# Kernel optimization log

Hardware: AMD Instinct MI355X
Metric: run time of the kernel (lower is better)

## Reference

```python
import jax, jax.numpy as jnp
import numpy as np

INPUT_DIM = 64
RESERVOIR_DIM = 2048
OUTPUT_DIM = 64
SPECTRAL_RADIUS = 0.9
LEAK_RATE = 0.3
SPARSITY = 0.9
INPUT_SCALING = 1.0
NOISE_LEVEL = 0.01
T = 4096


def setup_inputs() -> dict:
    key = jax.random.key(0)
    k_u, k_n = jax.random.split(key)
    u = jax.random.normal(k_u, (T, INPUT_DIM), dtype=jnp.float32)
    noise = jax.random.normal(k_n, (T, RESERVOIR_DIM), dtype=jnp.float32)

    # Reservoir weights, built exactly like the torch __init__ (fixed, untrained).
    rng = np.random.default_rng(0)
    W_in = (rng.standard_normal((RESERVOIR_DIM, INPUT_DIM)) * INPUT_SCALING).astype(np.float32)
    W = (rng.uniform(0.0, 1.0, (RESERVOIR_DIM, RESERVOIR_DIM)) * 2.0 - 1.0).astype(np.float32)
    mask = rng.uniform(0.0, 1.0, (RESERVOIR_DIM, RESERVOIR_DIM)) > SPARSITY
    W = W * mask.astype(np.float32)
    sr = np.max(np.abs(np.linalg.eigvals(W)))  # spectral radius normalization
    W = (W * (SPECTRAL_RADIUS / sr)).astype(np.float32)

    # nn.Linear(reservoir_dim, output_dim) init: U(-1/sqrt(N), 1/sqrt(N))
    bound = 1.0 / np.sqrt(RESERVOIR_DIM)
    readout_w = rng.uniform(-bound, bound, (OUTPUT_DIM, RESERVOIR_DIM)).astype(np.float32)
    readout_b = rng.uniform(-bound, bound, (OUTPUT_DIM,)).astype(np.float32)

    return {
        "u": u,
        "noise": noise,
        "W_in": jnp.asarray(W_in),
        "W": jnp.asarray(W),
        "readout_w": jnp.asarray(readout_w),
        "readout_b": jnp.asarray(readout_b),
    }


def reference(u, noise, W_in, W, readout_w, readout_b):
    # Leaky-integrated ESN recurrence, state reset to zeros (reset_state=True).
    input_terms = u @ W_in.T + noise * NOISE_LEVEL  # [T, N], precompute input GEMM

    def step(state, it):
        new_state = jnp.tanh(it + W @ state)
        state = (1.0 - LEAK_RATE) * state + LEAK_RATE * new_state
        return state, state

    init = jnp.zeros((RESERVOIR_DIM,), dtype=u.dtype)
    _, states = jax.lax.scan(step, init, input_terms)  # states: [T, N]
    return states @ readout_w.T + readout_b  # [T, output_dim]
```

## Files before the change

### kernel.cpp

```cpp
#include <hip/hip_runtime.h>

#define T_STEPS 4096
#define N_RES   2048
#define N_IN    64
#define N_OUT   64
#define LEAK    0.3f
#define NOISE_S 0.01f

#define NWG     128
#define RPW     16
#define RPWAVE  4

typedef unsigned int uint32x4 __attribute__((ext_vector_type(4)));

__global__ __launch_bounds__(256) void input_terms_kernel(
    const float* __restrict__ u, const float* __restrict__ noise,
    const float* __restrict__ W_in, float* __restrict__ it) {
  const int t = blockIdx.x;
  const int tid = threadIdx.x;
  __shared__ float su[N_IN];
  if (tid < N_IN) su[tid] = u[(size_t)t * N_IN + tid];
  __syncthreads();
  #pragma unroll
  for (int k = 0; k < N_RES / 256; ++k) {
    const int n = tid + 256 * k;
    const float4* wr = reinterpret_cast<const float4*>(W_in + (size_t)n * N_IN);
    float acc = 0.f;
    #pragma unroll
    for (int j = 0; j < N_IN / 4; ++j) {
      float4 w4 = wr[j];
      acc = fmaf(w4.x, su[4 * j + 0], acc);
      acc = fmaf(w4.y, su[4 * j + 1], acc);
      acc = fmaf(w4.z, su[4 * j + 2], acc);
      acc = fmaf(w4.w, su[4 * j + 3], acc);
    }
    it[(size_t)t * N_RES + n] = acc + NOISE_S * noise[(size_t)t * N_RES + n];
  }
}

__global__ __launch_bounds__(256, 1) void reservoir_kernel(
    const float* __restrict__ W, float* __restrict__ it,
    unsigned int* sbuf) {
  const int wg = blockIdx.x;
  const int tid = threadIdx.x;
  const int wave = tid >> 6;
  const int lane = tid & 63;
  const int R = wg * RPW;
  const int r0 = R + wave * RPWAVE;

  __shared__ float Wl[RPW * N_RES];
  __shared__ float ls[2][N_RES];

  {
    const float4* Wg = reinterpret_cast<const float4*>(W + (size_t)R * N_RES);
    float4* Wd = reinterpret_cast<float4*>(Wl);
    #pragma unroll
    for (int k = 0; k < RPW * N_RES / 4 / 256; ++k)
      Wd[tid + 256 * k] = Wg[tid + 256 * k];
  }

  float itv = 0.f;
  if (lane < RPWAVE) itv = it[r0 + lane];

  {
    const uint32x4* pa = reinterpret_cast<const uint32x4*>(sbuf) + tid;
    const uint32x4* pb = pa + 256;
    uint32x4* dsta = reinterpret_cast<uint32x4*>(&ls[0][0]) + tid;
    uint32x4* dstb = dsta + 256;
    unsigned int need = 3u;
    while (need) {
      uint32x4 va, vb;
      asm volatile(
          "global_load_dwordx4 %0, %2, off sc0 sc1\n\t"
          "global_load_dwordx4 %1, %3, off sc0 sc1\n\t"
          "s_waitcnt vmcnt(0)"
          : "=&v"(va), "=&v"(vb) : "v"(pa), "v"(pb) : "memory");
      if ((need & 1u) &&
          (((va[0] | va[1] | va[2] | va[3]) & 3u) == 0u)) { *dsta = va; need &= ~1u; }
      if ((need & 2u) &&
          (((vb[0] | vb[1] | vb[2] | vb[3]) & 3u) == 0u)) { *dstb = vb; need &= ~2u; }
      if (need) __builtin_amdgcn_s_sleep(1);
    }
  }
  __syncthreads();

  for (unsigned int t = 0; t < T_STEPS; ++t) {
    const float* cur = ls[t & 1];
    float* nxt = ls[(t + 1) & 1];
    unsigned int* swb = sbuf + ((t + 1) & 1) * N_RES;

    const float4* S4 = reinterpret_cast<const float4*>(cur);
    const float4* W0 = reinterpret_cast<const float4*>(Wl + (size_t)(RPWAVE * wave + 0) * N_RES);
    const float4* W1 = reinterpret_cast<const float4*>(Wl + (size_t)(RPWAVE * wave + 1) * N_RES);
    const float4* W2 = reinterpret_cast<const float4*>(Wl + (size_t)(RPWAVE * wave + 2) * N_RES);
    const float4* W3 = reinterpret_cast<const float4*>(Wl + (size_t)(RPWAVE * wave + 3) * N_RES);
    float a0 = 0.f, a1 = 0.f, a2 = 0.f, a3 = 0.f;
    #pragma unroll
    for (int j = 0; j < N_RES / 4 / 64; ++j) {
      const float4 s4 = S4[lane + 64 * j];
      const float4 x0 = W0[lane + 64 * j];
      const float4 x1 = W1[lane + 64 * j];
      const float4 x2 = W2[lane + 64 * j];
      const float4 x3 = W3[lane + 64 * j];
      a0 = fmaf(x0.x, s4.x, a0); a0 = fmaf(x0.y, s4.y, a0);
      a0 = fmaf(x0.z, s4.z, a0); a0 = fmaf(x0.w, s4.w, a0);
      a1 = fmaf(x1.x, s4.x, a1); a1 = fmaf(x1.y, s4.y, a1);
      a1 = fmaf(x1.z, s4.z, a1); a1 = fmaf(x1.w, s4.w, a1);
      a2 = fmaf(x2.x, s4.x, a2); a2 = fmaf(x2.y, s4.y, a2);
      a2 = fmaf(x2.z, s4.z, a2); a2 = fmaf(x2.w, s4.w, a2);
      a3 = fmaf(x3.x, s4.x, a3); a3 = fmaf(x3.y, s4.y, a3);
      a3 = fmaf(x3.z, s4.z, a3); a3 = fmaf(x3.w, s4.w, a3);
    }
    #pragma unroll
    for (int off = 32; off > 0; off >>= 1) {
      a0 += __shfl_xor(a0, off);
      a1 += __shfl_xor(a1, off);
      a2 += __shfl_xor(a2, off);
      a3 += __shfl_xor(a3, off);
    }

    float snew = 0.f;
    if (lane < RPWAVE) {
      const float a = (lane == 0) ? a0 : (lane == 1) ? a1 : (lane == 2) ? a2 : a3;
      const float h = tanhf(itv + a);
      const float sold = cur[r0 + lane];
      snew = (1.0f - LEAK) * sold + LEAK * h;
      it[(size_t)t * N_RES + r0 + lane] = snew;
    }

    {
      const unsigned int tg = (t + 1) & 3u;
      uint32x4 pk;
      pk[0] = (__float_as_uint(__shfl(snew, 0)) & ~3u) | tg;
      pk[1] = (__float_as_uint(__shfl(snew, 1)) & ~3u) | tg;
      pk[2] = (__float_as_uint(__shfl(snew, 2)) & ~3u) | tg;
      pk[3] = (__float_as_uint(__shfl(snew, 3)) & ~3u) | tg;
      if (lane == 0) {
        uint32x4* dst = reinterpret_cast<uint32x4*>(swb) + (r0 >> 2);
        asm volatile("global_store_dwordx4 %0, %1, off sc0 sc1"
                     :: "v"(dst), "v"(pk) : "memory");
      }
    }

    if (t + 1 < T_STEPS) {
      if (lane < RPWAVE) itv = it[(size_t)(t + 1) * N_RES + r0 + lane];

      const unsigned int tag = (t + 1) & 3u;
      const uint32x4* pa = reinterpret_cast<const uint32x4*>(swb) + tid;
      const uint32x4* pb = pa + 256;
      uint32x4* dsta = reinterpret_cast<uint32x4*>(nxt) + tid;
      uint32x4* dstb = dsta + 256;
      unsigned int need = 3u;
      for (;;) {
        uint32x4 va, vb;
        if (need == 3u) {
          asm volatile(
              "global_load_dwordx4 %0, %2, off sc0 sc1\n\t"
              "global_load_dwordx4 %1, %3, off sc0 sc1\n\t"
              "s_waitcnt vmcnt(0)"
              : "=&v"(va), "=&v"(vb) : "v"(pa), "v"(pb) : "memory");
          if ((((va[0] ^ tag) | (va[1] ^ tag) | (va[2] ^ tag) | (va[3] ^ tag)) & 3u) == 0u) {
            *dsta = va; need &= ~1u;
          }
          if ((((vb[0] ^ tag) | (vb[1] ^ tag) | (vb[2] ^ tag) | (vb[3] ^ tag)) & 3u) == 0u) {
            *dstb = vb; need &= ~2u;
          }
        } else if (need == 1u) {
          asm volatile(
              "global_load_dwordx4 %0, %1, off sc0 sc1\n\t"
              "s_waitcnt vmcnt(0)"
              : "=&v"(va) : "v"(pa) : "memory");
          if ((((va[0] ^ tag) | (va[1] ^ tag) | (va[2] ^ tag) | (va[3] ^ tag)) & 3u) == 0u) {
            *dsta = va; need = 0u;
          }
        } else {
          asm volatile(
              "global_load_dwordx4 %0, %1, off sc0 sc1\n\t"
              "s_waitcnt vmcnt(0)"
              : "=&v"(vb) : "v"(pb) : "memory");
          if ((((vb[0] ^ tag) | (vb[1] ^ tag) | (vb[2] ^ tag) | (vb[3] ^ tag)) & 3u) == 0u) {
            *dstb = vb; need = 0u;
          }
        }
        if (!need) break;
        __builtin_amdgcn_s_sleep(1);
      }
    }
    __syncthreads();
  }
}

__global__ __launch_bounds__(256) void readout_kernel(
    const float* __restrict__ states, const float* __restrict__ rw,
    const float* __restrict__ rb, float* __restrict__ out) {
  const int t = blockIdx.x;
  const int tid = threadIdx.x;
  const int o = tid & 63;
  const int q = tid >> 6;
  __shared__ float ss[N_RES];
  #pragma unroll
  for (int k = 0; k < N_RES / 256; ++k)
    ss[tid + 256 * k] = states[(size_t)t * N_RES + tid + 256 * k];
  __syncthreads();

  const float4* r4 = reinterpret_cast<const float4*>(rw + (size_t)o * N_RES + q * 512);
  float acc = 0.f;
  #pragma unroll 8
  for (int j = 0; j < 128; ++j) {
    float4 w4 = r4[j];
    const int base = q * 512 + 4 * j;
    acc = fmaf(w4.x, ss[base + 0], acc);
    acc = fmaf(w4.y, ss[base + 1], acc);
    acc = fmaf(w4.z, ss[base + 2], acc);
    acc = fmaf(w4.w, ss[base + 3], acc);
  }
  __shared__ float red[256];
  red[tid] = acc;
  __syncthreads();
  if (tid < 64) {
    float v = red[tid] + red[tid + 64] + red[tid + 128] + red[tid + 192];
    out[(size_t)t * N_OUT + tid] = v + rb[tid];
  }
}

extern "C" void kernel_launch(void* const* d_in, const int* in_sizes, int n_in,
                              void* d_out, int out_size, void* d_ws, size_t ws_size,
                              hipStream_t stream) {
  const float* u     = (const float*)d_in[0];
  const float* noise = (const float*)d_in[1];
  const float* W_in  = (const float*)d_in[2];
  const float* W     = (const float*)d_in[3];
  const float* rw    = (const float*)d_in[4];
  const float* rb    = (const float*)d_in[5];
  float* out = (float*)d_out;

  float* it = (float*)d_ws;
  unsigned int* sbuf =
      (unsigned int*)((char*)d_ws + (size_t)T_STEPS * N_RES * sizeof(float));

  hipMemsetAsync(sbuf, 0, 2 * N_RES * sizeof(unsigned int), stream);

  input_terms_kernel<<<T_STEPS, 256, 0, stream>>>(u, noise, W_in, it);

  void* args[] = {(void*)&W, (void*)&it, (void*)&sbuf};
  hipLaunchCooperativeKernel((void*)reservoir_kernel, dim3(NWG), dim3(256),
                             args, 0, stream);

  readout_kernel<<<T_STEPS, 256, 0, stream>>>(it, rw, rb, out);
}
```

Measured before the change: 13.63 ms.

## Add dedicated polling wave to gather peer states while compute waves run

Splits the reservoir workgroup into four compute waves and one extra wave that only polls the global exchange buffer. The poller issues all eight tagged loads per round and copies ready chunks into shared memory. Each compute wave writes its own new state straight into shared memory, so it skips polling its own chunk. The aim is to take the spin-wait off the compute waves and remove the redundant self-fetch. In exchange, one wave is serialized on polling and a block-wide barrier is still needed every step.

```diff
diff --git a/kernel.cpp b/kernel.cpp
--- a/kernel.cpp
+++ b/kernel.cpp
@@ -7,9 +7,10 @@
 #define LEAK    0.3f
 #define NOISE_S 0.01f
 
-#define NWG     128
-#define RPW     16
-#define RPWAVE  4
+#define NWG      128
+#define RPW      16
+#define RPWAVE   4
+#define NTHREADS 320
 
 typedef unsigned int uint32x4 __attribute__((ext_vector_type(4)));
 
@@ -38,7 +39,7 @@
   }
 }
 
-__global__ __launch_bounds__(256, 1) void reservoir_kernel(
+__global__ __launch_bounds__(NTHREADS, 1) void reservoir_kernel(
     const float* __restrict__ W, float* __restrict__ it,
     unsigned int* sbuf) {
   const int wg = blockIdx.x;
@@ -46,7 +47,6 @@
   const int wave = tid >> 6;
   const int lane = tid & 63;
   const int R = wg * RPW;
-  const int r0 = R + wave * RPWAVE;
 
   __shared__ float Wl[RPW * N_RES];
   __shared__ float ls[2][N_RES];
@@ -54,139 +54,124 @@
   {
     const float4* Wg = reinterpret_cast<const float4*>(W + (size_t)R * N_RES);
     float4* Wd = reinterpret_cast<float4*>(Wl);
-    #pragma unroll
-    for (int k = 0; k < RPW * N_RES / 4 / 256; ++k)
-      Wd[tid + 256 * k] = Wg[tid + 256 * k];
-  }
-
-  float itv = 0.f;
-  if (lane < RPWAVE) itv = it[r0 + lane];
-
-  {
-    const uint32x4* pa = reinterpret_cast<const uint32x4*>(sbuf) + tid;
-    const uint32x4* pb = pa + 256;
-    uint32x4* dsta = reinterpret_cast<uint32x4*>(&ls[0][0]) + tid;
-    uint32x4* dstb = dsta + 256;
-    unsigned int need = 3u;
-    while (need) {
-      uint32x4 va, vb;
-      asm volatile(
-          "global_load_dwordx4 %0, %2, off sc0 sc1\n\t"
-          "global_load_dwordx4 %1, %3, off sc0 sc1\n\t"
-          "s_waitcnt vmcnt(0)"
-          : "=&v"(va), "=&v"(vb) : "v"(pa), "v"(pb) : "memory");
-      if ((need & 1u) &&
-          (((va[0] | va[1] | va[2] | va[3]) & 3u) == 0u)) { *dsta = va; need &= ~1u; }
-      if ((need & 2u) &&
-          (((vb[0] | vb[1] | vb[2] | vb[3]) & 3u) == 0u)) { *dstb = vb; need &= ~2u; }
-      if (need) __builtin_amdgcn_s_sleep(1);
-    }
-  }
-  __syncthreads();
-
-  for (unsigned int t = 0; t < T_STEPS; ++t) {
-    const float* cur = ls[t & 1];
-    float* nxt = ls[(t + 1) & 1];
-    unsigned int* swb = sbuf + ((t + 1) & 1) * N_RES;
-
-    const float4* S4 = reinterpret_cast<const float4*>(cur);
+    for (int idx = tid; idx < RPW * N_RES / 4; idx += NTHREADS)
+      Wd[idx] = Wg[idx];
+  }
+  for (int idx = tid; idx < N_RES; idx += NTHREADS) ls[0][idx] = 0.f;
+  __syncthreads();
+
+  if (wave < 4) {
+    const int r0 = R + wave * RPWAVE;
     const float4* W0 = reinterpret_cast<const float4*>(Wl + (size_t)(RPWAVE * wave + 0) * N_RES);
     const float4* W1 = reinterpret_cast<const float4*>(Wl + (size_t)(RPWAVE * wave + 1) * N_RES);
     const float4* W2 = reinterpret_cast<const float4*>(Wl + (size_t)(RPWAVE * wave + 2) * N_RES);
     const float4* W3 = reinterpret_cast<const float4*>(Wl + (size_t)(RPWAVE * wave + 3) * N_RES);
-    float a0 = 0.f, a1 = 0.f, a2 = 0.f, a3 = 0.f;
-    #pragma unroll
-    for (int j = 0; j < N_RES / 4 / 64; ++j) {
-      const float4 s4 = S4[lane + 64 * j];
-      const float4 x0 = W0[lane + 64 * j];
-      const float4 x1 = W1[lane + 64 * j];
-      const float4 x2 = W2[lane + 64 * j];
-      const float4 x3 = W3[lane + 64 * j];
-      a0 = fmaf(x0.x, s4.x, a0); a0 = fmaf(x0.y, s4.y, a0);
-      a0 = fmaf(x0.z, s4.z, a0); a0 = fmaf(x0.w, s4.w, a0);
-      a1 = fmaf(x1.x, s4.x, a1); a1 = fmaf(x1.y, s4.y, a1);
-      a1 = fmaf(x1.z, s4.z, a1); a1 = fmaf(x1.w, s4.w, a1);
-      a2 = fmaf(x2.x, s4.x, a2); a2 = fmaf(x2.y, s4.y, a2);
-      a2 = fmaf(x2.z, s4.z, a2); a2 = fmaf(x2.w, s4.w, a2);
-      a3 = fmaf(x3.x, s4.x, a3); a3 = fmaf(x3.y, s4.y, a3);
-      a3 = fmaf(x3.z, s4.z, a3); a3 = fmaf(x3.w, s4.w, a3);
-    }
-    #pragma unroll
-    for (int off = 32; off > 0; off >>= 1) {
-      a0 += __shfl_xor(a0, off);
-      a1 += __shfl_xor(a1, off);
-      a2 += __shfl_xor(a2, off);
-      a3 += __shfl_xor(a3, off);
-    }
-
-    float snew = 0.f;
-    if (lane < RPWAVE) {
-      const float a = (lane == 0) ? a0 : (lane == 1) ? a1 : (lane == 2) ? a2 : a3;
-      const float h = tanhf(itv + a);
-      const float sold = cur[r0 + lane];
-      snew = (1.0f - LEAK) * sold + LEAK * h;
-      it[(size_t)t * N_RES + r0 + lane] = snew;
-    }
-
-    {
+
+    float itv = 0.f;
+    if (lane < RPWAVE) itv = it[r0 + lane];
+
+    for (unsigned int t = 0; t < T_STEPS; ++t) {
+      const float* cur = ls[t & 1];
+      float* nxt = ls[(t + 1) & 1];
+      unsigned int* swb = sbuf + ((t + 1) & 1) * N_RES;
+
+      const float4* S4 = reinterpret_cast<const float4*>(cur);
+      float a0 = 0.f, a1 = 0.f, a2 = 0.f, a3 = 0.f;
+      #pragma unroll
+      for (int j = 0; j < N_RES / 4 / 64; ++j) {
+        const float4 s4 = S4[lane + 64 * j];
+        const float4 x0 = W0[lane + 64 * j];
+        const float4 x1 = W1[lane + 64 * j];
+        const float4 x2 = W2[lane + 64 * j];
+        const float4 x3 = W3[lane + 64 * j];
+        a0 = fmaf(x0.x, s4.x, a0); a0 = fmaf(x0.y, s4.y, a0);
+        a0 = fmaf(x0.z, s4.z, a0); a0 = fmaf(x0.w, s4.w, a0);
+        a1 = fmaf(x1.x, s4.x, a1); a1 = fmaf(x1.y, s4.y, a1);
+        a1 = fmaf(x1.z, s4.z, a1); a1 = fmaf(x1.w, s4.w, a1);
+        a2 = fmaf(x2.x, s4.x, a2); a2 = fmaf(x2.y, s4.y, a2);
+        a2 = fmaf(x2.z, s4.z, a2); a2 = fmaf(x2.w, s4.w, a2);
+        a3 = fmaf(x3.x, s4.x, a3); a3 = fmaf(x3.y, s4.y, a3);
+        a3 = fmaf(x3.z, s4.z, a3); a3 = fmaf(x3.w, s4.w, a3);
+      }
+      #pragma unroll
+      for (int off = 32; off > 0; off >>= 1) {
+        a0 += __shfl_xor(a0, off);
+        a1 += __shfl_xor(a1, off);
+        a2 += __shfl_xor(a2, off);
+        a3 += __shfl_xor(a3, off);
+      }
+
       const unsigned int tg = (t + 1) & 3u;
+      unsigned int pkw = 0;
+      if (lane < RPWAVE) {
+        const float a = (lane == 0) ? a0 : (lane == 1) ? a1 : (lane == 2) ? a2 : a3;
+        const float h = tanhf(itv + a);
+        const float sold = cur[r0 + lane];
+        const float snew = (1.0f - LEAK) * sold + LEAK * h;
+        pkw = (__float_as_uint(snew) & ~3u) | tg;
+        nxt[r0 + lane] = __uint_as_float(pkw);
+        it[(size_t)t * N_RES + r0 + lane] = snew;
+      }
       uint32x4 pk;
-      pk[0] = (__float_as_uint(__shfl(snew, 0)) & ~3u) | tg;
-      pk[1] = (__float_as_uint(__shfl(snew, 1)) & ~3u) | tg;
-      pk[2] = (__float_as_uint(__shfl(snew, 2)) & ~3u) | tg;
-      pk[3] = (__float_as_uint(__shfl(snew, 3)) & ~3u) | tg;
+      pk[0] = __shfl(pkw, 0);
+      pk[1] = __shfl(pkw, 1);
+      pk[2] = __shfl(pkw, 2);
+      pk[3] = __shfl(pkw, 3);
       if (lane == 0) {
         uint32x4* dst = reinterpret_cast<uint32x4*>(swb) + (r0 >> 2);
         asm volatile("global_store_dwordx4 %0, %1, off sc0 sc1"
                      :: "v"(dst), "v"(pk) : "memory");
       }
-    }
-
-    if (t + 1 < T_STEPS) {
-      if (lane < RPWAVE) itv = it[(size_t)(t + 1) * N_RES + r0 + lane];
-
-      const unsigned int tag = (t + 1) & 3u;
-      const uint32x4* pa = reinterpret_cast<const uint32x4*>(swb) + tid;
-      const uint32x4* pb = pa + 256;
-      uint32x4* dsta = reinterpret_cast<uint32x4*>(nxt) + tid;
-      uint32x4* dstb = dsta + 256;
-      unsigned int need = 3u;
-      for (;;) {
-        uint32x4 va, vb;
-        if (need == 3u) {
+      if (lane < RPWAVE && t + 1 < T_STEPS)
+        itv = it[(size_t)(t + 1) * N_RES + r0 + lane];
+
+      __syncthreads();
+    }
+  } else {
+    unsigned int ownmask = 0;
+    {
+      const int j = lane - ((wg * 4) & 63);
+      if (0 <= j && j < 4) ownmask = 1u << (wg >> 4);
+    }
+    for (unsigned int t = 0; t < T_STEPS; ++t) {
+      if (t + 1 < T_STEPS) {
+        unsigned int* swb = sbuf + ((t + 1) & 1) * N_RES;
+        float* nxt = ls[(t + 1) & 1];
+        const unsigned int tg = (t + 1) & 3u;
+        const char* p0 = (const char*)swb + lane * 16;
+        const char* p1 = p0 + 4096;
+        uint32x4* dst = reinterpret_cast<uint32x4*>(nxt);
+        unsigned int need = 0xFFu & ~ownmask;
+        for (;;) {
+          uint32x4 v0, v1, v2, v3, v4, v5, v6, v7;
           asm volatile(
-              "global_load_dwordx4 %0, %2, off sc0 sc1\n\t"
-              "global_load_dwordx4 %1, %3, off sc0 sc1\n\t"
+              "global_load_dwordx4 %0, %8, off sc0 sc1\n\t"
+              "global_load_dwordx4 %1, %8, off offset:1024 sc0 sc1\n\t"
+              "global_load_dwordx4 %2, %8, off offset:2048 sc0 sc1\n\t"
+              "global_load_dwordx4 %3, %8, off offset:3072 sc0 sc1\n\t"
+              "global_load_dwordx4 %4, %9, off sc0 sc1\n\t"
+              "global_load_dwordx4 %5, %9, off offset:1024 sc0 sc1\n\t"
+              "global_load_dwordx4 %6, %9, off offset:2048 sc0 sc1\n\t"
+              "global_load_dwordx4 %7, %9, off offset:3072 sc0 sc1\n\t"
               "s_waitcnt vmcnt(0)"
-              : "=&v"(va), "=&v"(vb) : "v"(pa), "v"(pb) : "memory");
-          if ((((va[0] ^ tag) | (va[1] ^ tag) | (va[2] ^ tag) | (va[3] ^ tag)) & 3u) == 0u) {
-            *dsta = va; need &= ~1u;
-          }
-          if ((((vb[0] ^ tag) | (vb[1] ^ tag) | (vb[2] ^ tag) | (vb[3] ^ tag)) & 3u) == 0u) {
-            *dstb = vb; need &= ~2u;
-          }
-        } else if (need == 1u) {
-          asm volatile(
-              "global_load_dwordx4 %0, %1, off sc0 sc1\n\t"
-              "s_waitcnt vmcnt(0)"
-              : "=&v"(va) : "v"(pa) : "memory");
-          if ((((va[0] ^ tag) | (va[1] ^ tag) | (va[2] ^ tag) | (va[3] ^ tag)) & 3u) == 0u) {
-            *dsta = va; need = 0u;
-          }
-        } else {
-          asm volatile(
-              "global_load_dwordx4 %0, %1, off sc0 sc1\n\t"
-              "s_waitcnt vmcnt(0)"
-              : "=&v"(vb) : "v"(pb) : "memory");
-          if ((((vb[0] ^ tag) | (vb[1] ^ tag) | (vb[2] ^ tag) | (vb[3] ^ tag)) & 3u) == 0u) {
-            *dstb = vb; need = 0u;
-          }
+              : "=&v"(v0), "=&v"(v1), "=&v"(v2), "=&v"(v3),
+                "=&v"(v4), "=&v"(v5), "=&v"(v6), "=&v"(v7)
+              : "v"(p0), "v"(p1)
+              : "memory");
+          if ((need & 1u)   && ((((v0[0]^tg)|(v0[1]^tg)|(v0[2]^tg)|(v0[3]^tg))&3u)==0u)) { dst[lane +   0] = v0; need &= ~1u; }
+          if ((need & 2u)   && ((((v1[0]^tg)|(v1[1]^tg)|(v1[2]^tg)|(v1[3]^tg))&3u)==0u)) { dst[lane +  64] = v1; need &= ~2u; }
+          if ((need & 4u)   && ((((v2[0]^tg)|(v2[1]^tg)|(v2[2]^tg)|(v2[3]^tg))&3u)==0u)) { dst[lane + 128] = v2; need &= ~4u; }
+          if ((need & 8u)   && ((((v3[0]^tg)|(v3[1]^tg)|(v3[2]^tg)|(v3[3]^tg))&3u)==0u)) { dst[lane + 192] = v3; need &= ~8u; }
+          if ((need & 16u)  && ((((v4[0]^tg)|(v4[1]^tg)|(v4[2]^tg)|(v4[3]^tg))&3u)==0u)) { dst[lane + 256] = v4; need &= ~16u; }
+          if ((need & 32u)  && ((((v5[0]^tg)|(v5[1]^tg)|(v5[2]^tg)|(v5[3]^tg))&3u)==0u)) { dst[lane + 320] = v5; need &= ~32u; }
+          if ((need & 64u)  && ((((v6[0]^tg)|(v6[1]^tg)|(v6[2]^tg)|(v6[3]^tg))&3u)==0u)) { dst[lane + 384] = v6; need &= ~64u; }
+          if ((need & 128u) && ((((v7[0]^tg)|(v7[1]^tg)|(v7[2]^tg)|(v7[3]^tg))&3u)==0u)) { dst[lane + 448] = v7; need &= ~128u; }
+          if (__all(need == 0u)) break;
+          __builtin_amdgcn_s_sleep(1);
         }
-        if (!need) break;
-        __builtin_amdgcn_s_sleep(1);
-      }
-    }
-    __syncthreads();
+      }
+      __syncthreads();
+    }
   }
 }
 
@@ -243,7 +228,7 @@
   input_terms_kernel<<<T_STEPS, 256, 0, stream>>>(u, noise, W_in, it);
 
   void* args[] = {(void*)&W, (void*)&it, (void*)&sbuf};
-  hipLaunchCooperativeKernel((void*)reservoir_kernel, dim3(NWG), dim3(256),
+  hipLaunchCooperativeKernel((void*)reservoir_kernel, dim3(NWG), dim3(NTHREADS),
                              args, 0, stream);
 
   readout_kernel<<<T_STEPS, 256, 0, stream>>>(it, rw, rb, out);
```

New measurement: 13.11 ms. -3.9%, faster.

## Spread recurrence over 256 workgroups and skip polling own state chunk

Applied to the files above, without the earlier changes.

The persistent recurrence kernel now uses 256 workgroups of 8 rows each instead of 128 of 16, so each wave computes 2 rows and the per-step dot product per workgroup is halved. Each workgroup writes its own new state values straight into shared memory and skips polling the global chunk it produced. The initial poll of the global buffer is replaced by zeroing the local state. The price is twice as many workgroups taking part in the per-step global flag exchange, which raises synchronisation traffic and needs all 256 to be co-resident.

```diff
diff --git a/kernel.cpp b/kernel.cpp
--- a/kernel.cpp
+++ b/kernel.cpp
@@ -7,11 +7,12 @@
 #define LEAK    0.3f
 #define NOISE_S 0.01f
 
-#define NWG     128
-#define RPW     16
-#define RPWAVE  4
+#define NWG      256
+#define RPW      8
+#define RPWAVE   2
 
 typedef unsigned int uint32x4 __attribute__((ext_vector_type(4)));
+typedef unsigned int uint32x2 __attribute__((ext_vector_type(2)));
 
 __global__ __launch_bounds__(256) void input_terms_kernel(
     const float* __restrict__ u, const float* __restrict__ noise,
@@ -58,31 +59,18 @@
     for (int k = 0; k < RPW * N_RES / 4 / 256; ++k)
       Wd[tid + 256 * k] = Wg[tid + 256 * k];
   }
+  for (int idx = tid; idx < N_RES; idx += 256) ls[0][idx] = 0.f;
+  __syncthreads();
+
+  const float4* W0 = reinterpret_cast<const float4*>(Wl + (size_t)(RPWAVE * wave + 0) * N_RES);
+  const float4* W1 = reinterpret_cast<const float4*>(Wl + (size_t)(RPWAVE * wave + 1) * N_RES);
+
+  const bool own0 = ((tid >> 1) == wg);
+  const bool own1 = (((tid + 256) >> 1) == wg);
+  const unsigned int own_mask = (own0 ? 1u : 0u) | (own1 ? 2u : 0u);
 
   float itv = 0.f;
   if (lane < RPWAVE) itv = it[r0 + lane];
-
-  {
-    const uint32x4* pa = reinterpret_cast<const uint32x4*>(sbuf) + tid;
-    const uint32x4* pb = pa + 256;
-    uint32x4* dsta = reinterpret_cast<uint32x4*>(&ls[0][0]) + tid;
-    uint32x4* dstb = dsta + 256;
-    unsigned int need = 3u;
-    while (need) {
-      uint32x4 va, vb;
-      asm volatile(
-          "global_load_dwordx4 %0, %2, off sc0 sc1\n\t"
-          "global_load_dwordx4 %1, %3, off sc0 sc1\n\t"
-          "s_waitcnt vmcnt(0)"
-          : "=&v"(va), "=&v"(vb) : "v"(pa), "v"(pb) : "memory");
-      if ((need & 1u) &&
-          (((va[0] | va[1] | va[2] | va[3]) & 3u) == 0u)) { *dsta = va; need &= ~1u; }
-      if ((need & 2u) &&
-          (((vb[0] | vb[1] | vb[2] | vb[3]) & 3u) == 0u)) { *dstb = vb; need &= ~2u; }
-      if (need) __builtin_amdgcn_s_sleep(1);
-    }
-  }
-  __syncthreads();
 
   for (unsigned int t = 0; t < T_STEPS; ++t) {
     const float* cur = ls[t & 1];
@@ -90,100 +78,85 @@
     unsigned int* swb = sbuf + ((t + 1) & 1) * N_RES;
 
     const float4* S4 = reinterpret_cast<const float4*>(cur);
-    const float4* W0 = reinterpret_cast<const float4*>(Wl + (size_t)(RPWAVE * wave + 0) * N_RES);
-    const float4* W1 = reinterpret_cast<const float4*>(Wl + (size_t)(RPWAVE * wave + 1) * N_RES);
-    const float4* W2 = reinterpret_cast<const float4*>(Wl + (size_t)(RPWAVE * wave + 2) * N_RES);
-    const float4* W3 = reinterpret_cast<const float4*>(Wl + (size_t)(RPWAVE * wave + 3) * N_RES);
-    float a0 = 0.f, a1 = 0.f, a2 = 0.f, a3 = 0.f;
-    #pragma unroll
-    for (int j = 0; j < N_RES / 4 / 64; ++j) {
+    float a0 = 0.f, a1 = 0.f;
+    #pragma unroll
+    for (int j = 0; j < 8; ++j) {
       const float4 s4 = S4[lane + 64 * j];
       const float4 x0 = W0[lane + 64 * j];
       const float4 x1 = W1[lane + 64 * j];
-      const float4 x2 = W2[lane + 64 * j];
-      const float4 x3 = W3[lane + 64 * j];
       a0 = fmaf(x0.x, s4.x, a0); a0 = fmaf(x0.y, s4.y, a0);
       a0 = fmaf(x0.z, s4.z, a0); a0 = fmaf(x0.w, s4.w, a0);
       a1 = fmaf(x1.x, s4.x, a1); a1 = fmaf(x1.y, s4.y, a1);
       a1 = fmaf(x1.z, s4.z, a1); a1 = fmaf(x1.w, s4.w, a1);
-      a2 = fmaf(x2.x, s4.x, a2); a2 = fmaf(x2.y, s4.y, a2);
-      a2 = fmaf(x2.z, s4.z, a2); a2 = fmaf(x2.w, s4.w, a2);
-      a3 = fmaf(x3.x, s4.x, a3); a3 = fmaf(x3.y, s4.y, a3);
-      a3 = fmaf(x3.z, s4.z, a3); a3 = fmaf(x3.w, s4.w, a3);
     }
     #pragma unroll
     for (int off = 32; off > 0; off >>= 1) {
       a0 += __shfl_xor(a0, off);
       a1 += __shfl_xor(a1, off);
-      a2 += __shfl_xor(a2, off);
-      a3 += __shfl_xor(a3, off);
-    }
-
+    }
+
+    const unsigned int tg = (t + 1) & 3u;
+    unsigned int pkw = 0;
     float snew = 0.f;
     if (lane < RPWAVE) {
-      const float a = (lane == 0) ? a0 : (lane == 1) ? a1 : (lane == 2) ? a2 : a3;
+      const float a = lane ? a1 : a0;
       const float h = tanhf(itv + a);
       const float sold = cur[r0 + lane];
       snew = (1.0f - LEAK) * sold + LEAK * h;
+      pkw = (__float_as_uint(snew) & ~3u) | tg;
+      nxt[r0 + lane] = __uint_as_float(pkw);
+    }
+    uint32x2 pk;
+    pk[0] = __shfl(pkw, 0);
+    pk[1] = __shfl(pkw, 1);
+    if (lane == 0) {
+      uint32x2* dst = reinterpret_cast<uint32x2*>(swb + r0);
+      asm volatile("global_store_dwordx2 %0, %1, off sc0 sc1"
+                   :: "v"(dst), "v"(pk) : "memory");
+    }
+    if (lane < RPWAVE) {
       it[(size_t)t * N_RES + r0 + lane] = snew;
-    }
-
-    {
-      const unsigned int tg = (t + 1) & 3u;
-      uint32x4 pk;
-      pk[0] = (__float_as_uint(__shfl(snew, 0)) & ~3u) | tg;
-      pk[1] = (__float_as_uint(__shfl(snew, 1)) & ~3u) | tg;
-      pk[2] = (__float_as_uint(__shfl(snew, 2)) & ~3u) | tg;
-      pk[3] = (__float_as_uint(__shfl(snew, 3)) & ~3u) | tg;
-      if (lane == 0) {
-        uint32x4* dst = reinterpret_cast<uint32x4*>(swb) + (r0 >> 2);
-        asm volatile("global_store_dwordx4 %0, %1, off sc0 sc1"
-                     :: "v"(dst), "v"(pk) : "memory");
-      }
+      if (t + 1 < T_STEPS)
+        itv = it[(size_t)(t + 1) * N_RES + r0 + lane];
     }
 
     if (t + 1 < T_STEPS) {
-      if (lane < RPWAVE) itv = it[(size_t)(t + 1) * N_RES + r0 + lane];
-
-      const unsigned int tag = (t + 1) & 3u;
-      const uint32x4* pa = reinterpret_cast<const uint32x4*>(swb) + tid;
-      const uint32x4* pb = pa + 256;
-      uint32x4* dsta = reinterpret_cast<uint32x4*>(nxt) + tid;
-      uint32x4* dstb = dsta + 256;
-      unsigned int need = 3u;
-      for (;;) {
+      const char* p0 = (const char*)swb + tid * 16;
+      const char* p1 = p0 + 4096;
+      uint32x4* nxt16 = reinterpret_cast<uint32x4*>(nxt);
+      unsigned int need = 3u & ~own_mask;
+      while (need) {
         uint32x4 va, vb;
         if (need == 3u) {
           asm volatile(
               "global_load_dwordx4 %0, %2, off sc0 sc1\n\t"
               "global_load_dwordx4 %1, %3, off sc0 sc1\n\t"
               "s_waitcnt vmcnt(0)"
-              : "=&v"(va), "=&v"(vb) : "v"(pa), "v"(pb) : "memory");
-          if ((((va[0] ^ tag) | (va[1] ^ tag) | (va[2] ^ tag) | (va[3] ^ tag)) & 3u) == 0u) {
-            *dsta = va; need &= ~1u;
-          }
-          if ((((vb[0] ^ tag) | (vb[1] ^ tag) | (vb[2] ^ tag) | (vb[3] ^ tag)) & 3u) == 0u) {
-            *dstb = vb; need &= ~2u;
+              : "=&v"(va), "=&v"(vb) : "v"(p0), "v"(p1) : "memory");
+          if ((((va[0] ^ tg) | (va[1] ^ tg) | (va[2] ^ tg) | (va[3] ^ tg)) & 3u) == 0u) {
+            nxt16[tid] = va; need &= ~1u;
+          }
+          if ((((vb[0] ^ tg) | (vb[1] ^ tg) | (vb[2] ^ tg) | (vb[3] ^ tg)) & 3u) == 0u) {
+            nxt16[tid + 256] = vb; need &= ~2u;
           }
         } else if (need == 1u) {
           asm volatile(
               "global_load_dwordx4 %0, %1, off sc0 sc1\n\t"
               "s_waitcnt vmcnt(0)"
-              : "=&v"(va) : "v"(pa) : "memory");
-          if ((((va[0] ^ tag) | (va[1] ^ tag) | (va[2] ^ tag) | (va[3] ^ tag)) & 3u) == 0u) {
-            *dsta = va; need = 0u;
+              : "=&v"(va) : "v"(p0) : "memory");
+          if ((((va[0] ^ tg) | (va[1] ^ tg) | (va[2] ^ tg) | (va[3] ^ tg)) & 3u) == 0u) {
+            nxt16[tid] = va; need = 0u;
           }
         } else {
           asm volatile(
               "global_load_dwordx4 %0, %1, off sc0 sc1\n\t"
               "s_waitcnt vmcnt(0)"
-              : "=&v"(vb) : "v"(pb) : "memory");
-          if ((((vb[0] ^ tag) | (vb[1] ^ tag) | (vb[2] ^ tag) | (vb[3] ^ tag)) & 3u) == 0u) {
-            *dstb = vb; need = 0u;
+              : "=&v"(vb) : "v"(p1) : "memory");
+          if ((((vb[0] ^ tg) | (vb[1] ^ tg) | (vb[2] ^ tg) | (vb[3] ^ tg)) & 3u) == 0u) {
+            nxt16[tid + 256] = vb; need = 0u;
           }
         }
-        if (!need) break;
-        __builtin_amdgcn_s_sleep(1);
+        if (need) __builtin_amdgcn_s_sleep(1);
       }
     }
     __syncthreads();
```

Result: slower. 16.91 ms (+24.0%).
